# Kernel tuning notes

Hardware: AMD Instinct MI355X
Metric: run time of the kernel (lower is better)

Reference implementation:

```python
import jax, jax.numpy as jnp
import numpy as np

B, Q, K, D, H = 2, 1024, 4096, 1024, 16
DH = D // H
LN_EPS = 1e-5


def setup_inputs() -> dict:
    key = jax.random.key(0)
    ks = jax.random.split(key, 10)
    queries = jax.random.normal(ks[0], (B, Q, D), jnp.float32)
    keys = jax.random.normal(ks[1], (B, K, D), jnp.float32)
    values = jax.random.normal(ks[2], (B, K, D), jnp.float32)
    # 128 words of 8 query tokens each: boundaries 0,8,...,1024 (sorted, unique)
    word_boundaries = jnp.arange(0, Q + 1, 8, dtype=jnp.int32)  # [129]
    # monotone map from query positions to char/key positions in [0, K]
    char_boundaries = jnp.sort(jax.random.randint(ks[3], (Q,), 0, K + 1, dtype=jnp.int32))
    s = 0.02
    ln_gamma = jnp.ones((D,), jnp.float32)
    ln_beta = jnp.zeros((D,), jnp.float32)
    in_proj_w = jax.random.normal(ks[4], (3 * D, D), jnp.float32) * s
    in_proj_b = jnp.zeros((3 * D,), jnp.float32)
    out_w = jax.random.normal(ks[5], (D, D), jnp.float32) * s
    out_b = jnp.zeros((D,), jnp.float32)
    return dict(queries=queries, keys=keys, values=values,
                word_boundaries=word_boundaries, char_boundaries=char_boundaries,
                ln_gamma=ln_gamma, ln_beta=ln_beta,
                in_proj_w=in_proj_w, in_proj_b=in_proj_b,
                out_w=out_w, out_b=out_b)


def char_aware_mask(wb, cb, q_len, k_len):
    """Vectorized version of the per-word python loop.
    Float mask of 0/1 (PyTorch ADDS a float attn_mask to the scores)."""
    ws, we = wb[:-1], wb[1:]                     # word start/end in query coords [nW]
    nW = ws.shape[0]
    cs = cb[ws]                                  # char span start per word
    ce = cb[we - 1]                              # char span end per word
    q = jnp.arange(q_len)
    i = jnp.clip(jnp.searchsorted(wb, q, side='right') - 1, 0, nW - 1)  # word id per query row
    valid = (q >= ws[i]) & (q < we[i])           # rows actually written by the loop
    j = jnp.arange(k_len)[None, :]               # [1, K]
    in_char = (j >= cs[i][:, None]) & (j < ce[i][:, None])
    # prev word: keys [wb[i-1], wb[i]) (query-coord indices used on key axis, as in source)
    ps = ws[jnp.maximum(i - 1, 0)]
    in_prev = (i > 0)[:, None] & (j >= ps[:, None]) & (j < ws[i][:, None])
    # next word: keys [wb[i+1], wb[i+2])
    ns = we[i]
    ne = wb[jnp.minimum(i + 2, nW)]
    in_next = (i < nW - 1)[:, None] & (j >= ns[:, None]) & (j < ne[:, None])
    return (valid[:, None] & (in_char | in_prev | in_next)).astype(jnp.float32)


def reference(queries, keys, values, word_boundaries, char_boundaries,
              ln_gamma, ln_beta, in_proj_w, in_proj_b, out_w, out_b):
    b, q_len, d = queries.shape
    k_len = keys.shape[1]
    mask = char_aware_mask(word_boundaries, char_boundaries, q_len, k_len)  # [Q, K]
    # LayerNorm(queries)
    mu = jnp.mean(queries, axis=-1, keepdims=True)
    var = jnp.var(queries, axis=-1, keepdims=True)
    x = (queries - mu) * jax.lax.rsqrt(var + LN_EPS) * ln_gamma + ln_beta
    # MultiheadAttention(x, keys, values, attn_mask=mask) -- float mask added to logits
    wq, wk, wv = jnp.split(in_proj_w, 3, axis=0)
    bq, bk, bv = jnp.split(in_proj_b, 3)
    qh = (x @ wq.T + bq).reshape(b, q_len, H, DH)
    kh = (keys @ wk.T + bk).reshape(b, k_len, H, DH)
    vh = (values @ wv.T + bv).reshape(b, k_len, H, DH)
    scale = 1.0 / jnp.sqrt(jnp.asarray(DH, queries.dtype))
    scores = jnp.einsum('bqhd,bkhd->bhqk', qh * scale, kh) + mask[None, None]
    attn = jax.nn.softmax(scores, axis=-1)
    ctx = jnp.einsum('bhqk,bkhd->bqhd', attn, vh).reshape(b, q_len, d)
    out = ctx @ out_w.T + out_b
    # residual; dropout is identity at inference
    return queries + out
```

## Files before the change

kernel.cpp:

```cpp
#include <hip/hip_runtime.h>
#include <hip/hip_bf16.h>


typedef __attribute__((ext_vector_type(8))) short bf16x8;
typedef __attribute__((ext_vector_type(4))) float f32x4;
typedef __attribute__((ext_vector_type(16))) float f32x16;

#define L2E 1.44269504088896341f
#define CSCALE (0.125f * L2E)
#define NSPLIT 4

__device__ __forceinline__ short f2bf(float f) {
  __hip_bfloat16 h = __float2bfloat16(f);
  return reinterpret_cast<short&>(h);
}

__device__ __forceinline__ unsigned cvtpk(float a, float b) {
  unsigned r;
  asm("v_cvt_pk_bf16_f32 %0, %1, %2" : "=v"(r) : "v"(a), "v"(b));
  return r;
}

__device__ __forceinline__ float fexp2(float x) {
#if __has_builtin(__builtin_amdgcn_exp2f)
  return __builtin_amdgcn_exp2f(x);
#else
  float r;
  asm("v_exp_f32 %0, %1" : "=v"(r) : "v"(x));
  return r;
#endif
}

__device__ __forceinline__ void halfswap(unsigned a, unsigned b, unsigned& x, unsigned& y) {
#if __has_builtin(__builtin_amdgcn_permlane32_swap)
  auto r = __builtin_amdgcn_permlane32_swap(a, b, false, false);
  x = (unsigned)r[0];
  y = (unsigned)r[1];
#else
  unsigned ca = (unsigned)__shfl_xor((int)a, 32);
  unsigned cb = (unsigned)__shfl_xor((int)b, 32);
  bool h = ((threadIdx.x & 63) >> 5) != 0;
  x = h ? cb : a;
  y = h ? b : ca;
#endif
}

__device__ __forceinline__ void gload16(const void* g, void* l) {
  __builtin_amdgcn_global_load_lds(
      (const __attribute__((address_space(1))) void*)g,
      (__attribute__((address_space(3))) void*)l, 16, 0, 0);
}

template <int N>
__device__ __forceinline__ void pipe_barrier() {
  __builtin_amdgcn_sched_barrier(0);
  if constexpr (N == 6)
    asm volatile("s_waitcnt vmcnt(6) lgkmcnt(0)" ::: "memory");
  else if constexpr (N == 2)
    asm volatile("s_waitcnt vmcnt(2) lgkmcnt(0)" ::: "memory");
  else
    asm volatile("s_waitcnt vmcnt(0) lgkmcnt(0)" ::: "memory");
  __builtin_amdgcn_s_barrier();
  __builtin_amdgcn_sched_barrier(0);
}

__global__ __launch_bounds__(256) void prep_kernel(const float* __restrict__ w,
                                                   const float* __restrict__ o,
                                                   short* __restrict__ dw,
                                                   short* __restrict__ dof,
                                                   const float* __restrict__ x,
                                                   const float* __restrict__ gamma,
                                                   const float* __restrict__ beta,
                                                   short* __restrict__ xout,
                                                   const int* __restrict__ wb,
                                                   const int* __restrict__ cb,
                                                   int* __restrict__ iv) {
  const int blk = blockIdx.x;
  const int t = threadIdx.x;
  if (blk < 4096) {
    long i = ((long)blk * 256 + t) * 4;
    const float* s;
    short* d;
    if (i < 3145728) { s = w + i; d = dw + i; }
    else { s = o + (i - 3145728); d = dof + (i - 3145728); }
    float4 xv = *(const float4*)s;
    uint2 r;
    r.x = cvtpk(xv.x, xv.y);
    r.y = cvtpk(xv.z, xv.w);
    *(uint2*)d = r;
  } else if (blk < 6144) {
    const int row = blk - 4096;
    float4 v = ((const float4*)(x + (size_t)row * 1024))[t];
    float s = v.x + v.y + v.z + v.w;
    float ss = v.x * v.x + v.y * v.y + v.z * v.z + v.w * v.w;
#pragma unroll
    for (int d = 32; d; d >>= 1) { s += __shfl_xor(s, d); ss += __shfl_xor(ss, d); }
    __shared__ float red[8];
    int wv2 = t >> 6, lane = t & 63;
    if (lane == 0) { red[wv2] = s; red[4 + wv2] = ss; }
    __syncthreads();
    s = red[0] + red[1] + red[2] + red[3];
    ss = red[4] + red[5] + red[6] + red[7];
    float mean = s * (1.0f / 1024.0f);
    float var = ss * (1.0f / 1024.0f) - mean * mean;
    float rstd = rsqrtf(var + 1e-5f);
    float4 g = ((const float4*)gamma)[t];
    float4 b = ((const float4*)beta)[t];
    uint2 oo;
    oo.x = cvtpk((v.x - mean) * rstd * g.x + b.x, (v.y - mean) * rstd * g.y + b.y);
    oo.y = cvtpk((v.z - mean) * rstd * g.z + b.z, (v.w - mean) * rstd * g.w + b.w);
    ((uint2*)(xout + (size_t)row * 1024))[t] = oo;
  } else {
    int q = (blk - 6144) * 256 + t;
    if (q >= 1024) return;
    int cnt = 0;
    for (int k = 0; k < 129; ++k) cnt += (wb[k] <= q) ? 1 : 0;
    int i = cnt - 1;
    i = i < 0 ? 0 : (i > 127 ? 127 : i);
    bool valid = (q >= wb[i]) && (q < wb[i + 1]);
    int cs = 0, ce = 0, pl = 0, ph = 0, nl = 0, nh = 0;
    if (valid) {
      cs = cb[wb[i]];
      ce = cb[wb[i + 1] - 1];
      if (i > 0) { pl = wb[i - 1]; ph = wb[i]; }
      if (i < 127) { nl = wb[i + 1]; nh = wb[(i + 2 <= 128) ? i + 2 : 128]; }
    }
    int* p = iv + q * 8;
    p[0] = cs; p[1] = ce; p[2] = pl; p[3] = ph; p[4] = nl; p[5] = nh; p[6] = 0; p[7] = 0;
  }
}

__device__ __forceinline__ unsigned inrange3(int key, const int* p) {
  bool m = (key >= p[0] && key < p[1]) || (key >= p[2] && key < p[3]) ||
           (key >= p[4] && key < p[5]);
  return m ? 1u : 0u;
}

__global__ __launch_bounds__(256) void mask_frag_kernel(const int* __restrict__ iv,
                                                        uint4* __restrict__ pmf) {
  int idx = blockIdx.x * 256 + threadIdx.x;
  int lane = idx & 63;
  int wg = (idx >> 6) & 31;
  int t = idx >> 11;
  int l31 = lane & 31, hi = lane >> 5;
  uint4 o = {0u, 0u, 0u, 0u};
  if (!hi) {
    int key0 = t * 64 + l31, key1 = key0 + 32;
    const int* p0 = iv + (wg * 32 + 0) * 8;
    const int* p1 = iv + (wg * 32 + 8) * 8;
    const int* p2 = iv + (wg * 32 + 16) * 8;
    const int* p3 = iv + (wg * 32 + 24) * 8;
    unsigned b0 = inrange3(key0, p0), b1 = inrange3(key0, p1);
    unsigned b2 = inrange3(key0, p2), b3 = inrange3(key0, p3);
    o.x = (b0 | (b1 << 16)) * 0x3F80u;
    o.y = (b2 | (b3 << 16)) * 0x3F80u;
    b0 = inrange3(key1, p0); b1 = inrange3(key1, p1);
    b2 = inrange3(key1, p2); b3 = inrange3(key1, p3);
    o.z = (b0 | (b1 << 16)) * 0x3F80u;
    o.w = (b2 | (b3 << 16)) * 0x3F80u;
  }
  pmf[idx] = o;
}

template <int AF32>
__device__ __forceinline__ void gemmKV_body(short* lds,
                                            const void* __restrict__ Aptr,
                                            const void* __restrict__ Wptr,
                                            const float* __restrict__ bias,
                                            void* __restrict__ Cout, int mode,
                                            int bx, int by) {
  const int lane = threadIdx.x & 63;
  const int w = threadIdx.x >> 6;
  const int m0 = bx * 128;
  const int n0 = by * 128;
  const int wm = w >> 1, wn = w & 1;
  const int l16 = lane & 15, lhi = lane >> 4;

  const int gc8 = (lane & 7) ^ (lane >> 3);
  const int lr = lane >> 3;
  const int rsw = (l16 & 7) << 4;

  const short* Bbf = AF32 ? (const short*)Wptr : (const short*)Aptr;
  const float* Ffp = AF32 ? (const float*)Aptr : (const float*)Wptr;
  const int fbase = AF32 ? m0 : n0;
  const int bbase = AF32 ? n0 : m0;
  short* bufF = lds;
  short* bufG = lds + 16384;

  f32x4 zero = {0.f, 0.f, 0.f, 0.f};
  f32x4 acc[2][4];
#pragma unroll
  for (int i = 0; i < 2; ++i)
#pragma unroll
    for (int j = 0; j < 4; ++j) acc[i][j] = zero;

  const int tid = (int)threadIdx.x;

  float4 xa[3][4];
  auto LOADF = [&](int k0, int slot) {
#pragma unroll
    for (int p = 0; p < 4; ++p) {
      int flat = p * 512 + tid;
      int row = flat >> 4, v4 = flat & 15;
      xa[slot][p] = *(const float4*)(Ffp + (size_t)(fbase + row) * 1024 + k0 + v4 * 4);
    }
  };
  auto WRITEF = [&](int slot, short* dst) {
#pragma unroll
    for (int p = 0; p < 4; ++p) {
      int flat = p * 512 + tid;
      int row = flat >> 4, v4 = flat & 15;
      uint2 u;
      u.x = cvtpk(xa[slot][p].x, xa[slot][p].y);
      u.y = cvtpk(xa[slot][p].z, xa[slot][p].w);
      *(uint2*)((char*)dst + row * 128 + ((v4 * 8) ^ ((row & 7) << 4))) = u;
    }
  };
  auto GLOADB = [&](int k0, short* dst) {
#pragma unroll
    for (int j = 0; j < 2; ++j) {
      int c = w * 2 + j;
      gload16(Bbf + (size_t)(bbase + c * 8 + lr) * 1024 + k0 + gc8 * 8, dst + c * 512);
    }
  };
  auto COMPUTE = [&](const short* cA, const short* cB) {
    bf16x8 af[2][2], bfr[4][2];
#pragma unroll
    for (int mt = 0; mt < 2; ++mt)
#pragma unroll
      for (int kk = 0; kk < 2; ++kk)
        af[mt][kk] = *(const bf16x8*)((const char*)cA + (wm * 32 + mt * 16 + l16) * 128 +
                                      ((kk * 64 + lhi * 16) ^ rsw));
#pragma unroll
    for (int nt = 0; nt < 4; ++nt)
#pragma unroll
      for (int kk = 0; kk < 2; ++kk)
        bfr[nt][kk] = *(const bf16x8*)((const char*)cB + (wn * 64 + nt * 16 + l16) * 128 +
                                       ((kk * 64 + lhi * 16) ^ rsw));
#pragma unroll
    for (int kk = 0; kk < 2; ++kk)
#pragma unroll
      for (int mt = 0; mt < 2; ++mt)
#pragma unroll
        for (int nt = 0; nt < 4; ++nt)
          acc[mt][nt] = __builtin_amdgcn_mfma_f32_16x16x32_bf16(af[mt][kk], bfr[nt][kk],
                                                                acc[mt][nt], 0, 0, 0);
  };

  LOADF(0, 0);
  GLOADB(0, bufG);
  WRITEF(0, bufF);
  LOADF(64, 1);
  GLOADB(64, bufG + 8192);
  LOADF(128, 2);
  pipe_barrier<6>();

#pragma unroll
  for (int k = 0; k < 16; ++k) {
    if (k + 3 < 16) LOADF((k + 3) * 64, (k + 3) % 3);
    if (k + 2 < 16) GLOADB((k + 2) * 64, bufG + ((k + 2) % 3) * 8192);
    if (k + 1 < 16) WRITEF((k + 1) % 3, bufF + ((k + 1) % 2) * 8192);
    if (AF32)
      COMPUTE(bufF + (k % 2) * 8192, bufG + (k % 3) * 8192);
    else
      COMPUTE(bufG + (k % 3) * 8192, bufF + (k % 2) * 8192);
    if (k <= 12) pipe_barrier<6>();
    else if (k == 13) pipe_barrier<2>();
    else if (k == 14) pipe_barrier<0>();
  }

#pragma unroll
  for (int mt = 0; mt < 2; ++mt)
#pragma unroll
    for (int nt = 0; nt < 4; ++nt) {
      int col = n0 + wn * 64 + nt * 16 + l16;
#pragma unroll
      for (int r = 0; r < 4; ++r) {
        int row = m0 + wm * 32 + mt * 16 + lhi * 4 + r;
        if (mode == 1) {
          float v = acc[mt][nt][r] + bias[row];
          int hh = row >> 6, dhl = row & 63;
          int bb = col >> 12, key = col & 4095;
          ((short*)Cout)[((size_t)((bb * 16 + hh) * 64 + dhl)) * 4096 + key] = f2bf(v);
        } else {
          float v = acc[mt][nt][r] + bias[col];
          int bb = row >> 12, key = row & 4095;
          int hh = col >> 6, dhl = col & 63;
          ((short*)Cout)[((size_t)((bb * 16 + hh) * 4096 + key)) * 64 + dhl] = f2bf(v);
        }
      }
    }
}

__device__ __forceinline__ void gemmQO_body(short* lA, short* lB,
                                            const short* __restrict__ A,
                                            const short* __restrict__ W,
                                            const float* __restrict__ bias,
                                            const float* __restrict__ resid,
                                            void* __restrict__ Cout, int mode,
                                            float scale, int bxi, int byi) {
  const int lane = threadIdx.x & 63;
  const int w = threadIdx.x >> 6;
  const int m0 = bxi * 64;
  const int n0 = byi * 128;
  const int wm = w >> 2, wn = w & 3;
  const int l16 = lane & 15, lhi = lane >> 4;

  const int gc8 = (lane & 7) ^ (lane >> 3);
  const int lr = lane >> 3;
  const int rsw = (l16 & 7) << 4;

  f32x4 zero = {0.f, 0.f, 0.f, 0.f};
  f32x4 acc[2][2];
#pragma unroll
  for (int i = 0; i < 2; ++i)
#pragma unroll
    for (int j = 0; j < 2; ++j) acc[i][j] = zero;

  for (int k0 = 0; k0 < 1024; k0 += 64) {
    __syncthreads();
#pragma unroll
    for (int j = 0; j < 3; ++j) {
      int c = w * 3 + j;
      if (c < 8)
        gload16(A + (size_t)(m0 + c * 8 + lr) * 1024 + k0 + gc8 * 8, &lA[c * 512]);
      else
        gload16(W + (size_t)(n0 + (c - 8) * 8 + lr) * 1024 + k0 + gc8 * 8,
                &lB[(c - 8) * 512]);
    }
    __syncthreads();
    bf16x8 af[2][2], bfr[2][2];
#pragma unroll
    for (int mt = 0; mt < 2; ++mt)
#pragma unroll
      for (int kk = 0; kk < 2; ++kk)
        af[mt][kk] = *(const bf16x8*)((const char*)lA + (wm * 32 + mt * 16 + l16) * 128 +
                                      ((kk * 64 + lhi * 16) ^ rsw));
#pragma unroll
    for (int nt = 0; nt < 2; ++nt)
#pragma unroll
      for (int kk = 0; kk < 2; ++kk)
        bfr[nt][kk] = *(const bf16x8*)((const char*)lB + (wn * 32 + nt * 16 + l16) * 128 +
                                       ((kk * 64 + lhi * 16) ^ rsw));
#pragma unroll
    for (int kk = 0; kk < 2; ++kk)
#pragma unroll
      for (int mt = 0; mt < 2; ++mt)
#pragma unroll
        for (int nt = 0; nt < 2; ++nt)
          acc[mt][nt] = __builtin_amdgcn_mfma_f32_16x16x32_bf16(af[mt][kk], bfr[nt][kk],
                                                                acc[mt][nt], 0, 0, 0);
  }

#pragma unroll
  for (int mt = 0; mt < 2; ++mt)
#pragma unroll
    for (int nt = 0; nt < 2; ++nt) {
      int col = n0 + wn * 32 + nt * 16 + l16;
      float bs = bias[col];
#pragma unroll
      for (int r = 0; r < 4; ++r) {
        int row = m0 + wm * 32 + mt * 16 + lhi * 4 + r;
        float v = acc[mt][nt][r] + bs;
        if (mode == 0) {
          ((short*)Cout)[(size_t)row * 1024 + col] = f2bf(v * scale);
        } else {
          size_t idx = (size_t)row * 1024 + col;
          ((float*)Cout)[idx] = v + resid[idx];
        }
      }
    }
}

__global__ __launch_bounds__(512, 4) void megaGemm_kernel(const float* __restrict__ keys,
                                                          const short* __restrict__ wk,
                                                          const float* __restrict__ kbias,
                                                          const short* __restrict__ wv,
                                                          const float* __restrict__ values,
                                                          const float* __restrict__ vbias,
                                                          short* __restrict__ khp,
                                                          short* __restrict__ vhT,
                                                          const short* __restrict__ xb,
                                                          const short* __restrict__ wq,
                                                          const float* __restrict__ qbias,
                                                          short* __restrict__ qhb) {
  __shared__ __attribute__((aligned(16))) short lds[40960];
  int id = blockIdx.x;
  if (id < 512) {
    gemmKV_body<1>(lds, keys, wk, kbias, khp, 3, id & 63, id >> 6);
  } else if (id < 1024) {
    int i2 = id - 512;
    gemmKV_body<0>(lds, wv, values, vbias, vhT, 1, i2 >> 6, i2 & 63);
  } else {
    int i2 = id - 1024;
    gemmQO_body(lds, lds + 4096, xb, wq, qbias, nullptr, qhb, 0, CSCALE, i2 & 31, i2 >> 5);
  }
}

__global__ __launch_bounds__(512, 4) void gemmQO_kernel(const short* __restrict__ A,
                                                        const short* __restrict__ W,
                                                        const float* __restrict__ bias,
                                                        const float* __restrict__ resid,
                                                        void* __restrict__ Cout, int mode,
                                                        float scale) {
  __shared__ __attribute__((aligned(16))) short lA[4096];
  __shared__ __attribute__((aligned(16))) short lB[8192];
  gemmQO_body(lA, lB, A, W, bias, resid, Cout, mode, scale, blockIdx.x, blockIdx.y);
}

__global__ __launch_bounds__(256) void attn9_kernel(const short* __restrict__ qh,
                                                    const short* __restrict__ khp,
                                                    const short* __restrict__ vtp,
                                                    const uint4* __restrict__ pmf,
                                                    short* __restrict__ pacc,
                                                    float* __restrict__ pml) {
  const int tid = threadIdx.x;
  const int lane = tid & 63;
  const int w = tid >> 6;
  const int l31 = lane & 31;
  const int hi = lane >> 5;
  const int id = blockIdx.x;
  const int qb = id >> 7;
  const int g = id & 127;
  const int bh = g >> 2;
  const int ks = g & 3;
  const int b = bh >> 4, h = bh & 15;

  __shared__ __attribute__((aligned(16))) short sK[2][4096];
  __shared__ __attribute__((aligned(16))) short sV[2][4096];

  const int wq0 = qb * 128 + w * 32;
  const int qrow = wq0 + l31;
  bf16x8 qf0, qf1, qf2, qf3;
  {
    const short* qp = qh + ((size_t)(b * 1024 + qrow)) * 1024 + h * 64 + hi * 8;
    qf0 = *(const bf16x8*)(qp);
    qf1 = *(const bf16x8*)(qp + 16);
    qf2 = *(const bf16x8*)(qp + 32);
    qf3 = *(const bf16x8*)(qp + 48);
  }

  bf16x8 bmv;
  {
    union { unsigned u[4]; bf16x8 v; } t;
    t.u[0] = t.u[1] = t.u[2] = t.u[3] = 0;
    int lj = l31 >> 3;
    unsigned val = 0x3FB9u << (16 * (lj & 1));
    if (!hi) t.u[lj >> 1] = val;
    bmv = t.v;
  }

  bf16x8 bones;
  {
    union { unsigned u[4]; bf16x8 v; } t;
    t.u[0] = t.u[1] = t.u[2] = t.u[3] = 0x3F803F80u;
    bones = t.v;
  }

  f32x16 fzero;
#pragma unroll
  for (int i = 0; i < 16; ++i) fzero[i] = 0.f;

  const int kchunk = ks * 1024;
  const int sub = (lane & 7) ^ (lane >> 3);
  const int r8 = lane >> 3;
  const size_t kbase_g = ((size_t)bh * 4096 + kchunk) * 64;
  const size_t vbase_g = ((size_t)bh * 64) * 4096 + (size_t)kchunk;
  const uint4* pmfp = pmf + ((size_t)(ks * 16) * 32 + qb * 4 + w) * 64 + lane;

  f32x16 acc0, acc1, acc2;
#pragma unroll
  for (int i = 0; i < 16; ++i) { acc0[i] = 0.f; acc1[i] = 0.f; acc2[i] = 0.f; }

  const int koff_swz = (lane & 7) << 4;

  auto STAGE = [&](int buf, int t) {
    int kt = t * 64;
#pragma unroll
    for (int q2 = 0; q2 < 2; ++q2) {
      int ch = w * 2 + q2;
      gload16(khp + kbase_g + (size_t)(kt + ch * 8 + r8) * 64 + sub * 8,
              (short*)sK[buf] + ch * 512);
      gload16(vtp + vbase_g + (size_t)(ch * 8 + r8) * 4096 + kt + sub * 8,
              (short*)sV[buf] + ch * 512);
    }
  };

  uint4 mf_cur = pmfp[0];
  uint4 mf_next = mf_cur;
  STAGE(0, 0);
  __syncthreads();
  int buf = 0;

  for (int t = 0; t < 16; ++t) {
    if (t < 15) {
      STAGE(buf ^ 1, t + 1);
      mf_next = pmfp[(size_t)(t + 1) * 2048];
    }

    bf16x8 am0, am1;
    {
      union { unsigned u[4]; bf16x8 v; } f;
      f.u[0] = mf_cur.x; f.u[1] = mf_cur.y; f.u[2] = 0; f.u[3] = 0;
      am0 = f.v;
      f.u[0] = mf_cur.z; f.u[1] = mf_cur.w;
      am1 = f.v;
    }

    __builtin_amdgcn_s_setprio(1);
    f32x16 ss0 = __builtin_amdgcn_mfma_f32_32x32x16_bf16(am0, bmv, fzero, 0, 0, 0);
    f32x16 ss1 = __builtin_amdgcn_mfma_f32_32x32x16_bf16(am1, bmv, fzero, 0, 0, 0);
#pragma unroll
    for (int c = 0; c < 4; ++c) {
      int off = (c * 32 + hi * 16) ^ koff_swz;
      bf16x8 k0 = *(const bf16x8*)((const char*)sK[buf] + l31 * 128 + off);
      bf16x8 k1 = *(const bf16x8*)((const char*)sK[buf] + (32 + l31) * 128 + off);
      bf16x8 qc = (c == 0) ? qf0 : (c == 1) ? qf1 : (c == 2) ? qf2 : qf3;
      ss0 = __builtin_amdgcn_mfma_f32_32x32x16_bf16(k0, qc, ss0, 0, 0, 0);
      ss1 = __builtin_amdgcn_mfma_f32_32x32x16_bf16(k1, qc, ss1, 0, 0, 0);
    }
    __builtin_amdgcn_s_setprio(0);

#pragma unroll
    for (int r = 0; r < 16; ++r) {
      ss0[r] = fexp2(ss0[r]);
      ss1[r] = fexp2(ss1[r]);
    }

    bf16x8 pa0, pa1, pa2, pa3;
    {
      unsigned a01 = cvtpk(ss0[0], ss0[1]), a23 = cvtpk(ss0[2], ss0[3]);
      unsigned a45 = cvtpk(ss0[4], ss0[5]), a67 = cvtpk(ss0[6], ss0[7]);
      unsigned a89 = cvtpk(ss0[8], ss0[9]), aAB = cvtpk(ss0[10], ss0[11]);
      unsigned aCD = cvtpk(ss0[12], ss0[13]), aEF = cvtpk(ss0[14], ss0[15]);
      union { unsigned u[4]; bf16x8 v; } f;
      halfswap(a01, a45, f.u[0], f.u[2]);
      halfswap(a23, a67, f.u[1], f.u[3]);
      pa0 = f.v;
      halfswap(a89, aCD, f.u[0], f.u[2]);
      halfswap(aAB, aEF, f.u[1], f.u[3]);
      pa1 = f.v;
    }
    {
      unsigned a01 = cvtpk(ss1[0], ss1[1]), a23 = cvtpk(ss1[2], ss1[3]);
      unsigned a45 = cvtpk(ss1[4], ss1[5]), a67 = cvtpk(ss1[6], ss1[7]);
      unsigned a89 = cvtpk(ss1[8], ss1[9]), aAB = cvtpk(ss1[10], ss1[11]);
      unsigned aCD = cvtpk(ss1[12], ss1[13]), aEF = cvtpk(ss1[14], ss1[15]);
      union { unsigned u[4]; bf16x8 v; } f;
      halfswap(a01, a45, f.u[0], f.u[2]);
      halfswap(a23, a67, f.u[1], f.u[3]);
      pa2 = f.v;
      halfswap(a89, aCD, f.u[0], f.u[2]);
      halfswap(aAB, aEF, f.u[1], f.u[3]);
      pa3 = f.v;
    }

    __builtin_amdgcn_s_setprio(1);
#pragma unroll
    for (int kb16 = 0; kb16 < 4; ++kb16) {
      int off = (kb16 * 32 + hi * 16) ^ koff_swz;
      bf16x8 v0 = *(const bf16x8*)((const char*)sV[buf] + l31 * 128 + off);
      bf16x8 v1 = *(const bf16x8*)((const char*)sV[buf] + (32 + l31) * 128 + off);
      bf16x8 pa = (kb16 == 0) ? pa0 : (kb16 == 1) ? pa1 : (kb16 == 2) ? pa2 : pa3;
      acc0 = __builtin_amdgcn_mfma_f32_32x32x16_bf16(pa, v0, acc0, 0, 0, 0);
      acc1 = __builtin_amdgcn_mfma_f32_32x32x16_bf16(pa, v1, acc1, 0, 0, 0);
      acc2 = __builtin_amdgcn_mfma_f32_32x32x16_bf16(pa, bones, acc2, 0, 0, 0);
    }
    __builtin_amdgcn_s_setprio(0);
    __syncthreads();
    buf ^= 1;
    mf_cur = mf_next;
  }

  short* paccp = pacc + (((size_t)ks * 32 + bh) * 1024) * 64;
#pragma unroll
  for (int r = 0; r < 16; r += 2) {
    int q0 = wq0 + ((r & 3) + 8 * (r >> 2)) + 4 * hi;
    int q1 = wq0 + (((r + 1) & 3) + 8 * ((r + 1) >> 2)) + 4 * hi;
    unsigned u0 = cvtpk(acc0[r], acc0[r + 1]);
    unsigned u1 = cvtpk(acc1[r], acc1[r + 1]);
    paccp[(size_t)q0 * 64 + l31] = (short)(u0 & 0xffffu);
    paccp[(size_t)q1 * 64 + l31] = (short)(u0 >> 16);
    paccp[(size_t)q0 * 64 + 32 + l31] = (short)(u1 & 0xffffu);
    paccp[(size_t)q1 * 64 + 32 + l31] = (short)(u1 >> 16);
  }
  if (l31 == 0) {
    float* mlp = pml + ((size_t)ks * 32 + bh) * 1024;
#pragma unroll
    for (int r = 0; r < 16; ++r) {
      int q = wq0 + ((r & 3) + 8 * (r >> 2)) + 4 * hi;
      mlp[q] = acc2[r];
    }
  }
}

__global__ __launch_bounds__(256) void combine_kernel(const short* __restrict__ pacc,
                                                      const float* __restrict__ pml,
                                                      short* __restrict__ ctx) {
  int idx = blockIdx.x * 256 + threadIdx.x;
  int dh4 = idx & 15;
  int row = idx >> 4;
  int bh = row >> 10, q = row & 1023;
  float L = 0.f, o0 = 0.f, o1 = 0.f, o2 = 0.f, o3 = 0.f;
#pragma unroll
  for (int k = 0; k < NSPLIT; ++k) {
    L += pml[((size_t)k * 32 + bh) * 1024 + q];
    uint2 u = *(const uint2*)&pacc[(((size_t)k * 32 + bh) * 1024 + q) * 64 + dh4 * 4];
    unsigned a = u.x, b2 = u.y;
    unsigned t0 = a << 16, t1 = a & 0xffff0000u, t2 = b2 << 16, t3 = b2 & 0xffff0000u;
    o0 += reinterpret_cast<float&>(t0);
    o1 += reinterpret_cast<float&>(t1);
    o2 += reinterpret_cast<float&>(t2);
    o3 += reinterpret_cast<float&>(t3);
  }
  float inv = 1.0f / L;
  uint2 st;
  st.x = cvtpk(o0 * inv, o1 * inv);
  st.y = cvtpk(o2 * inv, o3 * inv);
  int b = bh >> 4, h = bh & 15;
  *(uint2*)&ctx[((size_t)(b * 1024 + q)) * 1024 + h * 64 + dh4 * 4] = st;
}

extern "C" void kernel_launch(void* const* d_in, const int* in_sizes, int n_in,
                              void* d_out, int out_size, void* d_ws, size_t ws_size,
                              hipStream_t stream) {
  const float* queries = (const float*)d_in[0];
  const float* keys    = (const float*)d_in[1];
  const float* values  = (const float*)d_in[2];
  const int*   wb      = (const int*)d_in[3];
  const int*   cb      = (const int*)d_in[4];
  const float* gamma   = (const float*)d_in[5];
  const float* beta    = (const float*)d_in[6];
  const float* ipw     = (const float*)d_in[7];
  const float* ipb     = (const float*)d_in[8];
  const float* ow      = (const float*)d_in[9];
  const float* ob      = (const float*)d_in[10];
  float* out = (float*)d_out;

  char* p = (char*)d_ws;
  short* xb  = (short*)p; p += (size_t)2048 * 1024 * 2;
  short* kb  = (short*)p; p += (size_t)8192 * 1024 * 2;
  short* vb  = (short*)p; p += (size_t)8192 * 1024 * 2;
  short* wpb = (short*)p; p += (size_t)3072 * 1024 * 2;
  short* owb = (short*)p; p += (size_t)1024 * 1024 * 2;
  short* qhb = (short*)p; p += (size_t)2048 * 1024 * 2;
  short* khp = (short*)p; p += (size_t)8192 * 1024 * 2;
  short* vhT = (short*)p; p += (size_t)8192 * 1024 * 2;
  short* ctx = (short*)p; p += (size_t)2048 * 1024 * 2;
  int* iv = (int*)p; p += (size_t)1024 * 8 * 4;
  uint4* pmf = (uint4*)p; p += (size_t)64 * 32 * 64 * 16;
  if ((size_t)(p - (char*)d_ws) > ws_size) return;
  (void)vb;

  short* pacc = kb;
  float* pml  = (float*)wpb;

  prep_kernel<<<6148, 256, 0, stream>>>(ipw, ow, wpb, owb, queries, gamma, beta, xb,
                                        wb, cb, iv);
  mask_frag_kernel<<<512, 256, 0, stream>>>(iv, pmf);

  megaGemm_kernel<<<1280, 512, 0, stream>>>(keys, wpb + 1048576, ipb + 1024,
                                            wpb + 2097152, values, ipb + 2048,
                                            khp, vhT, xb, wpb, ipb, qhb);

  attn9_kernel<<<1024, 256, 0, stream>>>(qhb, khp, vhT, pmf, pacc, pml);
  combine_kernel<<<2048, 256, 0, stream>>>(pacc, pml, ctx);

  gemmQO_kernel<<<dim3(32, 8), 512, 0, stream>>>(ctx, owb, ob, queries, out, 2, 1.f);
}
```

Measured before the change: 148.7 us.

## Pre-convert K/V to bf16 and use 256x256 tiled KV projection GEMM

Moves the fp32-to-bf16 conversion of keys and values into the prep kernel, writing bf16 copies to workspace. The K/V projection GEMM is then rewritten with 256x256 tiles loaded via direct global-to-LDS loads, double-buffered, with 8x4 MFMA tiles per wave. The goal is more data reuse per tile and removal of register-staged fp32 conversion from the GEMM inner loop. The cost is an extra full read and write pass over K/V, 128KB of LDS per block, and a launch bound lowered to 2 blocks per CU.

New measurement: 151.4 us. No clear change (+1.9%).

```diff
diff --git a/kernel.cpp b/kernel.cpp
--- a/kernel.cpp
+++ b/kernel.cpp
@@ -54,12 +54,20 @@
 template <int N>
 __device__ __forceinline__ void pipe_barrier() {
   __builtin_amdgcn_sched_barrier(0);
-  if constexpr (N == 6)
+  if constexpr (N == 8)
+    asm volatile("s_waitcnt vmcnt(8) lgkmcnt(0)" ::: "memory");
+  else if constexpr (N == 6)
     asm volatile("s_waitcnt vmcnt(6) lgkmcnt(0)" ::: "memory");
   else if constexpr (N == 2)
     asm volatile("s_waitcnt vmcnt(2) lgkmcnt(0)" ::: "memory");
   else
     asm volatile("s_waitcnt vmcnt(0) lgkmcnt(0)" ::: "memory");
+  __builtin_amdgcn_s_barrier();
+  __builtin_amdgcn_sched_barrier(0);
+}
+
+__device__ __forceinline__ void lds_barrier() {
+  __builtin_amdgcn_sched_barrier(0);
   __builtin_amdgcn_s_barrier();
   __builtin_amdgcn_sched_barrier(0);
 }
@@ -74,7 +82,11 @@
                                                    short* __restrict__ xout,
                                                    const int* __restrict__ wb,
                                                    const int* __restrict__ cb,
-                                                   int* __restrict__ iv) {
+                                                   int* __restrict__ iv,
+                                                   const float* __restrict__ keys,
+                                                   const float* __restrict__ values,
+                                                   short* __restrict__ kbf,
+                                                   short* __restrict__ vbf) {
   const int blk = blockIdx.x;
   const int t = threadIdx.x;
   if (blk < 4096) {
@@ -110,7 +122,7 @@
     oo.x = cvtpk((v.x - mean) * rstd * g.x + b.x, (v.y - mean) * rstd * g.y + b.y);
     oo.y = cvtpk((v.z - mean) * rstd * g.z + b.z, (v.w - mean) * rstd * g.w + b.w);
     ((uint2*)(xout + (size_t)row * 1024))[t] = oo;
-  } else {
+  } else if (blk < 6148) {
     int q = (blk - 6144) * 256 + t;
     if (q >= 1024) return;
     int cnt = 0;
@@ -127,6 +139,17 @@
     }
     int* p = iv + q * 8;
     p[0] = cs; p[1] = ce; p[2] = pl; p[3] = ph; p[4] = nl; p[5] = nh; p[6] = 0; p[7] = 0;
+  } else {
+    long i = ((long)(blk - 6148) * 256 + t) * 4;
+    const float* s;
+    short* d;
+    if (i < 8388608) { s = keys + i; d = kbf + i; }
+    else { s = values + (i - 8388608); d = vbf + (i - 8388608); }
+    float4 xv = *(const float4*)s;
+    uint2 r;
+    r.x = cvtpk(xv.x, xv.y);
+    r.y = cvtpk(xv.z, xv.w);
+    *(uint2*)d = r;
   }
 }
 
@@ -162,131 +185,89 @@
   pmf[idx] = o;
 }
 
-template <int AF32>
-__device__ __forceinline__ void gemmKV_body(short* lds,
-                                            const void* __restrict__ Aptr,
-                                            const void* __restrict__ Wptr,
-                                            const float* __restrict__ bias,
-                                            void* __restrict__ Cout, int mode,
-                                            int bx, int by) {
-  const int lane = threadIdx.x & 63;
-  const int w = threadIdx.x >> 6;
-  const int m0 = bx * 128;
-  const int n0 = by * 128;
-  const int wm = w >> 1, wn = w & 1;
+__device__ __forceinline__ void kv256_body(short* lds, const short* __restrict__ Agl,
+                                           const short* __restrict__ Bgl,
+                                           const float* __restrict__ bias,
+                                           short* __restrict__ Cout, int mode,
+                                           int bx, int by) {
+  const int tid = (int)threadIdx.x;
+  const int lane = tid & 63;
+  const int w = tid >> 6;
+  const int wm = w >> 2, wn = w & 3;
   const int l16 = lane & 15, lhi = lane >> 4;
-
   const int gc8 = (lane & 7) ^ (lane >> 3);
   const int lr = lane >> 3;
   const int rsw = (l16 & 7) << 4;
-
-  const short* Bbf = AF32 ? (const short*)Wptr : (const short*)Aptr;
-  const float* Ffp = AF32 ? (const float*)Aptr : (const float*)Wptr;
-  const int fbase = AF32 ? m0 : n0;
-  const int bbase = AF32 ? n0 : m0;
-  short* bufF = lds;
-  short* bufG = lds + 16384;
-
-  f32x4 zero = {0.f, 0.f, 0.f, 0.f};
-  f32x4 acc[2][4];
-#pragma unroll
-  for (int i = 0; i < 2; ++i)
-#pragma unroll
-    for (int j = 0; j < 4; ++j) acc[i][j] = zero;
-
-  const int tid = (int)threadIdx.x;
-
-  float4 xa[3][4];
-  auto LOADF = [&](int k0, int slot) {
-#pragma unroll
-    for (int p = 0; p < 4; ++p) {
-      int flat = p * 512 + tid;
-      int row = flat >> 4, v4 = flat & 15;
-      xa[slot][p] = *(const float4*)(Ffp + (size_t)(fbase + row) * 1024 + k0 + v4 * 4);
+  const int m0 = bx * 256, n0 = by * 256;
+
+  f32x4 acc[8][4];
+#pragma unroll
+  for (int i = 0; i < 8; ++i)
+#pragma unroll
+    for (int j = 0; j < 4; ++j) acc[i][j] = f32x4{0.f, 0.f, 0.f, 0.f};
+
+  auto STAGE = [&](int t, int bsel) {
+    const int k0 = t * 64;
+    short* dA = lds + bsel * 32768;
+    short* dB = dA + 16384;
+#pragma unroll
+    for (int j = 0; j < 4; ++j) {
+      int ch = w * 4 + j;
+      gload16(Agl + (size_t)(m0 + ch * 8 + lr) * 1024 + k0 + gc8 * 8, dA + ch * 512);
+      gload16(Bgl + (size_t)(n0 + ch * 8 + lr) * 1024 + k0 + gc8 * 8, dB + ch * 512);
     }
   };
-  auto WRITEF = [&](int slot, short* dst) {
-#pragma unroll
-    for (int p = 0; p < 4; ++p) {
-      int flat = p * 512 + tid;
-      int row = flat >> 4, v4 = flat & 15;
-      uint2 u;
-      u.x = cvtpk(xa[slot][p].x, xa[slot][p].y);
-      u.y = cvtpk(xa[slot][p].z, xa[slot][p].w);
-      *(uint2*)((char*)dst + row * 128 + ((v4 * 8) ^ ((row & 7) << 4))) = u;
+
+  auto COMPUTE = [&](int bsel) {
+    const char* cA = (const char*)(lds + bsel * 32768);
+    const char* cB = cA + 32768;
+#pragma unroll
+    for (int kk = 0; kk < 2; ++kk) {
+      bf16x8 af[8], bfr[4];
+#pragma unroll
+      for (int mt = 0; mt < 8; ++mt)
+        af[mt] = *(const bf16x8*)(cA + (wm * 128 + mt * 16 + l16) * 128 +
+                                  ((kk * 64 + lhi * 16) ^ rsw));
+#pragma unroll
+      for (int nt = 0; nt < 4; ++nt)
+        bfr[nt] = *(const bf16x8*)(cB + (wn * 64 + nt * 16 + l16) * 128 +
+                                   ((kk * 64 + lhi * 16) ^ rsw));
+#pragma unroll
+      for (int mt = 0; mt < 8; ++mt)
+#pragma unroll
+        for (int nt = 0; nt < 4; ++nt)
+          acc[mt][nt] = __builtin_amdgcn_mfma_f32_16x16x32_bf16(af[mt], bfr[nt],
+                                                                acc[mt][nt], 0, 0, 0);
     }
   };
-  auto GLOADB = [&](int k0, short* dst) {
-#pragma unroll
-    for (int j = 0; j < 2; ++j) {
-      int c = w * 2 + j;
-      gload16(Bbf + (size_t)(bbase + c * 8 + lr) * 1024 + k0 + gc8 * 8, dst + c * 512);
-    }
-  };
-  auto COMPUTE = [&](const short* cA, const short* cB) {
-    bf16x8 af[2][2], bfr[4][2];
-#pragma unroll
-    for (int mt = 0; mt < 2; ++mt)
-#pragma unroll
-      for (int kk = 0; kk < 2; ++kk)
-        af[mt][kk] = *(const bf16x8*)((const char*)cA + (wm * 32 + mt * 16 + l16) * 128 +
-                                      ((kk * 64 + lhi * 16) ^ rsw));
-#pragma unroll
-    for (int nt = 0; nt < 4; ++nt)
-#pragma unroll
-      for (int kk = 0; kk < 2; ++kk)
-        bfr[nt][kk] = *(const bf16x8*)((const char*)cB + (wn * 64 + nt * 16 + l16) * 128 +
-                                       ((kk * 64 + lhi * 16) ^ rsw));
-#pragma unroll
-    for (int kk = 0; kk < 2; ++kk)
-#pragma unroll
-      for (int mt = 0; mt < 2; ++mt)
-#pragma unroll
-        for (int nt = 0; nt < 4; ++nt)
-          acc[mt][nt] = __builtin_amdgcn_mfma_f32_16x16x32_bf16(af[mt][kk], bfr[nt][kk],
-                                                                acc[mt][nt], 0, 0, 0);
-  };
-
-  LOADF(0, 0);
-  GLOADB(0, bufG);
-  WRITEF(0, bufF);
-  LOADF(64, 1);
-  GLOADB(64, bufG + 8192);
-  LOADF(128, 2);
-  pipe_barrier<6>();
-
-#pragma unroll
-  for (int k = 0; k < 16; ++k) {
-    if (k + 3 < 16) LOADF((k + 3) * 64, (k + 3) % 3);
-    if (k + 2 < 16) GLOADB((k + 2) * 64, bufG + ((k + 2) % 3) * 8192);
-    if (k + 1 < 16) WRITEF((k + 1) % 3, bufF + ((k + 1) % 2) * 8192);
-    if (AF32)
-      COMPUTE(bufF + (k % 2) * 8192, bufG + (k % 3) * 8192);
-    else
-      COMPUTE(bufG + (k % 3) * 8192, bufF + (k % 2) * 8192);
-    if (k <= 12) pipe_barrier<6>();
-    else if (k == 13) pipe_barrier<2>();
-    else if (k == 14) pipe_barrier<0>();
-  }
-
-#pragma unroll
-  for (int mt = 0; mt < 2; ++mt)
+
+  STAGE(0, 0);
+  STAGE(1, 1);
+  for (int t = 0; t < 15; ++t) {
+    pipe_barrier<8>();
+    COMPUTE(t & 1);
+    lds_barrier();
+    if (t < 14) STAGE(t + 2, t & 1);
+  }
+  pipe_barrier<0>();
+  COMPUTE(1);
+
+#pragma unroll
+  for (int mt = 0; mt < 8; ++mt)
 #pragma unroll
     for (int nt = 0; nt < 4; ++nt) {
-      int col = n0 + wn * 64 + nt * 16 + l16;
+      int n = n0 + wn * 64 + nt * 16 + l16;
 #pragma unroll
       for (int r = 0; r < 4; ++r) {
-        int row = m0 + wm * 32 + mt * 16 + lhi * 4 + r;
-        if (mode == 1) {
-          float v = acc[mt][nt][r] + bias[row];
-          int hh = row >> 6, dhl = row & 63;
-          int bb = col >> 12, key = col & 4095;
-          ((short*)Cout)[((size_t)((bb * 16 + hh) * 64 + dhl)) * 4096 + key] = f2bf(v);
+        int m = m0 + wm * 128 + mt * 16 + lhi * 4 + r;
+        float v = acc[mt][nt][r];
+        if (mode == 0) {
+          int bb = m >> 12, key = m & 4095;
+          int hh = n >> 6, dhl = n & 63;
+          Cout[((size_t)((bb * 16 + hh) * 4096 + key)) * 64 + dhl] = f2bf(v + bias[n]);
         } else {
-          float v = acc[mt][nt][r] + bias[col];
-          int bb = row >> 12, key = row & 4095;
-          int hh = col >> 6, dhl = col & 63;
-          ((short*)Cout)[((size_t)((bb * 16 + hh) * 4096 + key)) * 64 + dhl] = f2bf(v);
+          int bb = n >> 12, key = n & 4095;
+          Cout[((size_t)(bb * 1024 + m)) * 4096 + key] = f2bf(v + bias[m]);
         }
       }
     }
@@ -372,11 +353,11 @@
     }
 }
 
-__global__ __launch_bounds__(512, 4) void megaGemm_kernel(const float* __restrict__ keys,
+__global__ __launch_bounds__(512, 2) void megaGemm_kernel(const short* __restrict__ kbf,
                                                           const short* __restrict__ wk,
                                                           const float* __restrict__ kbias,
                                                           const short* __restrict__ wv,
-                                                          const float* __restrict__ values,
+                                                          const short* __restrict__ vbf,
                                                           const float* __restrict__ vbias,
                                                           short* __restrict__ khp,
                                                           short* __restrict__ vhT,
@@ -384,15 +365,15 @@
                                                           const short* __restrict__ wq,
                                                           const float* __restrict__ qbias,
                                                           short* __restrict__ qhb) {
-  __shared__ __attribute__((aligned(16))) short lds[40960];
+  __shared__ __attribute__((aligned(16))) short lds[65536];
   int id = blockIdx.x;
-  if (id < 512) {
-    gemmKV_body<1>(lds, keys, wk, kbias, khp, 3, id & 63, id >> 6);
-  } else if (id < 1024) {
-    int i2 = id - 512;
-    gemmKV_body<0>(lds, wv, values, vbias, vhT, 1, i2 >> 6, i2 & 63);
+  if (id < 128) {
+    kv256_body(lds, kbf, wk, kbias, khp, 0, id & 31, id >> 5);
+  } else if (id < 256) {
+    int i2 = id & 127;
+    kv256_body(lds, wv, vbf, vbias, vhT, 1, i2 >> 5, i2 & 31);
   } else {
-    int i2 = id - 1024;
+    int i2 = id - 256;
     gemmQO_body(lds, lds + 4096, xb, wq, qbias, nullptr, qhb, 0, CSCALE, i2 & 31, i2 >> 5);
   }
 }
@@ -650,18 +631,17 @@
   int* iv = (int*)p; p += (size_t)1024 * 8 * 4;
   uint4* pmf = (uint4*)p; p += (size_t)64 * 32 * 64 * 16;
   if ((size_t)(p - (char*)d_ws) > ws_size) return;
-  (void)vb;
 
   short* pacc = kb;
   float* pml  = (float*)wpb;
 
-  prep_kernel<<<6148, 256, 0, stream>>>(ipw, ow, wpb, owb, queries, gamma, beta, xb,
-                                        wb, cb, iv);
+  prep_kernel<<<22532, 256, 0, stream>>>(ipw, ow, wpb, owb, queries, gamma, beta, xb,
+                                         wb, cb, iv, keys, values, kb, vb);
   mask_frag_kernel<<<512, 256, 0, stream>>>(iv, pmf);
 
-  megaGemm_kernel<<<1280, 512, 0, stream>>>(keys, wpb + 1048576, ipb + 1024,
-                                            wpb + 2097152, values, ipb + 2048,
-                                            khp, vhT, xb, wpb, ipb, qhb);
+  megaGemm_kernel<<<512, 512, 0, stream>>>(kb, wpb + 1048576, ipb + 1024,
+                                           wpb + 2097152, vb, ipb + 2048,
+                                           khp, vhT, xb, wpb, ipb, qhb);
 
   attn9_kernel<<<1024, 256, 0, stream>>>(qhb, khp, vhT, pmf, pacc, pml);
   combine_kernel<<<2048, 256, 0, stream>>>(pacc, pml, ctx);
```
